# Kernel tuning notes

Hardware: AMD Instinct MI355X
Metric: run time of the kernel (lower is better)

Reference implementation:

```python
import jax, jax.numpy as jnp
import numpy as np

B, H, S, D = 4, 16, 2048, 128


def setup_inputs() -> dict:
    key = jax.random.key(0)
    kq, kk, kv = jax.random.split(key, 3)
    query = jax.random.normal(kq, (B, H, S, D), dtype=jnp.float32)
    key_t = jax.random.normal(kk, (B, H, S, D), dtype=jnp.float32)
    value = jax.random.normal(kv, (B, H, S, D), dtype=jnp.float32)
    # causal mask, broadcast over batch and heads: True = keep
    mask = jnp.tril(jnp.ones((S, S), dtype=bool))[None, None].repeat(B, 0).repeat(H, 1)
    return {"query": query, "key": key_t, "value": value, "mask": mask}


def reference(query, key, value, mask):
    scale = 1.0 / np.sqrt(D).astype(np.float32)
    # [b,h,sq,sk] scores
    scores = jnp.einsum("bhqd,bhkd->bhqk", query, key) * scale
    scores = jnp.where(mask, scores, -jnp.inf)
    probs = jax.nn.softmax(scores, axis=-1)
    return jnp.einsum("bhqk,bhkd->bhqd", probs, value)
```

## Files before the change

kernel.cpp:

```cpp
#include <hip/hip_runtime.h>


#define SLEN 2048
#define DDIM 128
#define NBH  64
#define QB   256
#define KB   64
#define NITEMS 512

typedef __bf16 bf16x8 __attribute__((ext_vector_type(8)));
typedef float  f32x16 __attribute__((ext_vector_type(16)));
typedef float  f32x4  __attribute__((ext_vector_type(4)));
typedef unsigned uint32x4 __attribute__((ext_vector_type(4)));
typedef unsigned short ushort_t;
typedef ushort_t ushort8 __attribute__((ext_vector_type(8)));

__device__ inline ushort_t f2bf(float f) {
  union { float f; unsigned u; } v; v.f = f;
  unsigned u = v.u;
  u += 0x7FFFu + ((u >> 16) & 1u);
  return (ushort_t)(u >> 16);
}

__device__ inline unsigned cvtpk_bf16(float lo, float hi) {
  unsigned r;
  asm("v_cvt_pk_bf16_f32 %0, %1, %2" : "=v"(r) : "v"(lo), "v"(hi));
  return r;
}

__device__ inline float exp2_fast(float x) {
  float r;
  asm("v_exp_f32 %0, %1" : "=v"(r) : "v"(x));
  return r;
}

__global__ __launch_bounds__(256) void prepass_kernel(
    const float* __restrict__ K, const float* __restrict__ V,
    ushort_t* __restrict__ Kb, ushort_t* __restrict__ Vt,
    int* __restrict__ cnt) {
  __shared__ float t[64][33];
  if (blockIdx.x == 0 && threadIdx.x == 0) *cnt = 0;
  if (blockIdx.x < 2048) {
    const int n4 = (int)((size_t)NBH * SLEN * DDIM / 4);
    const int stride = 2048 * 256;
    for (int i = blockIdx.x * 256 + threadIdx.x; i < n4; i += stride) {
      float4 x = reinterpret_cast<const float4*>(K)[i];
      unsigned lo = (unsigned)f2bf(x.x) | ((unsigned)f2bf(x.y) << 16);
      unsigned hi = (unsigned)f2bf(x.z) | ((unsigned)f2bf(x.w) << 16);
      reinterpret_cast<uint2*>(Kb)[i] = make_uint2(lo, hi);
    }
  } else {
    const int vb = (int)blockIdx.x - 2048;
    const int bh = vb >> 7;
    const int d0 = ((vb >> 5) & 3) * 32;
    const int s0 = (vb & 31) * 64;
    const int tx = threadIdx.x & 31;
    const int ty = threadIdx.x >> 5;
    const float* src = V + ((size_t)bh * SLEN + s0) * DDIM + d0;
#pragma unroll
    for (int j = 0; j < 8; ++j) {
      int sl = ty + j * 8;
      t[sl][tx] = src[(size_t)sl * DDIM + tx];
    }
    __syncthreads();
    ushort_t* dst = Vt + ((size_t)bh * DDIM + d0) * SLEN + s0;
#pragma unroll
    for (int j = 0; j < 4; ++j) {
      int dl = ty + j * 8;
      unsigned lo = f2bf(t[tx * 2][dl]);
      unsigned hi = f2bf(t[tx * 2 + 1][dl]);
      *reinterpret_cast<unsigned*>(&dst[(size_t)dl * SLEN + tx * 2]) =
          lo | (hi << 16);
    }
  }
}

__global__ __launch_bounds__(512, 1) void fattn11_kernel(
    const float* __restrict__ Q, const ushort_t* __restrict__ Kb,
    const ushort_t* __restrict__ Vt, float* __restrict__ Out,
    int* __restrict__ cnt) {
  __shared__ ushort_t K_sh[3][KB * DDIM];
  __shared__ ushort_t V_sh[3][DDIM * KB];
  __shared__ int item_sh;

  const int tid  = threadIdx.x;
  const int lane = tid & 63;
  const int wv   = tid >> 6;
  const int l31  = lane & 31;
  const int hi   = lane >> 5;

  const float qscale = 0.12751744f;
  const float THR = 11.0f;

  while (true) {
    if (tid == 0) item_sh = atomicAdd(cnt, 1);
    __syncthreads();
    const int item = item_sh;
    if (item >= NITEMS) break;

    const int qblk = 7 - (item >> 6);
    const int bh   = item & 63;

    const float*    Qp = Q  + (size_t)bh * SLEN * DDIM;
    const ushort_t* Kp = Kb + (size_t)bh * SLEN * DDIM;
    const ushort_t* Vp = Vt + (size_t)bh * DDIM * SLEN;
    float*          Op = Out + (size_t)bh * SLEN * DDIM;

    const int q0w = qblk * QB + wv * 32;
    const int qg  = q0w + l31;

    bf16x8 qf[8];
    {
      const float* qr = Qp + (size_t)qg * DDIM;
#pragma unroll
      for (int ds = 0; ds < 8; ++ds) {
        int d0 = ds * 16 + hi * 8;
        float4 x = *reinterpret_cast<const float4*>(qr + d0);
        float4 y = *reinterpret_cast<const float4*>(qr + d0 + 4);
        ushort8 uu;
        uu[0] = f2bf(x.x * qscale); uu[1] = f2bf(x.y * qscale);
        uu[2] = f2bf(x.z * qscale); uu[3] = f2bf(x.w * qscale);
        uu[4] = f2bf(y.x * qscale); uu[5] = f2bf(y.y * qscale);
        uu[6] = f2bf(y.z * qscale); uu[7] = f2bf(y.w * qscale);
        qf[ds] = __builtin_bit_cast(bf16x8, uu);
      }
    }

    f32x16 Oacc[4];
#pragma unroll
    for (int dt = 0; dt < 4; ++dt)
#pragma unroll
      for (int r = 0; r < 16; ++r) Oacc[dt][r] = 0.f;
    float m_run = -3.0e38f, l_run = 0.f;

    const int last_kb      = qblk * 4 + 3;
    const int last_kb_wave = (q0w + 31) >> 6;

    auto stage = [&](int buf, int kb) {
      const ushort_t* ksrc = Kp + (size_t)kb * KB * DDIM;
#pragma unroll
      for (int j = 0; j < 2; ++j) {
        int chunk = wv * 128 + j * 64 + lane;
        int row = chunk >> 4, c = chunk & 15;
        const ushort_t* g = ksrc + row * DDIM + ((c ^ (row & 7)) << 3);
        ushort_t* l = &K_sh[buf][(wv * 128 + j * 64) * 8];
        __builtin_amdgcn_global_load_lds(
            (const __attribute__((address_space(1))) unsigned*)g,
            (__attribute__((address_space(3))) unsigned*)l, 16, 0, 0);
      }
      const ushort_t* vsrc = Vp + (size_t)kb * KB;
#pragma unroll
      for (int j = 0; j < 2; ++j) {
        int chunk = wv * 128 + j * 64 + lane;
        int row = chunk >> 3, c = chunk & 7;
        const ushort_t* g = vsrc + (size_t)row * SLEN + ((c ^ (row & 7)) << 3);
        ushort_t* l = &V_sh[buf][(wv * 128 + j * 64) * 8];
        __builtin_amdgcn_global_load_lds(
            (const __attribute__((address_space(1))) unsigned*)g,
            (__attribute__((address_space(3))) unsigned*)l, 16, 0, 0);
      }
    };

    stage(0, 0);
    stage(1, 1);
    asm volatile("s_waitcnt vmcnt(4)" ::: "memory");
    __builtin_amdgcn_s_barrier();
    __builtin_amdgcn_sched_barrier(0);

    for (int kb = 0; kb <= last_kb; ++kb) {
      const int buf = kb % 3;
      const bool pf = (kb + 2 <= last_kb);
      if (pf) stage((kb + 2) % 3, kb + 2);

      if (kb <= last_kb_wave) {
        f32x16 sac[2];
#pragma unroll
        for (int mt = 0; mt < 2; ++mt) {
          f32x16 a;
#pragma unroll
          for (int r = 0; r < 16; ++r) a[r] = 0.f;
          int row = mt * 32 + l31;
          int sw = row & 7;
          __builtin_amdgcn_s_setprio(1);
#pragma unroll
          for (int ds = 0; ds < 8; ++ds) {
            int c = ds * 2 + hi;
            bf16x8 kf = *reinterpret_cast<const bf16x8*>(
                &K_sh[buf][row * DDIM + ((c ^ sw) << 3)]);
            a = __builtin_amdgcn_mfma_f32_32x32x16_bf16(kf, qf[ds], a, 0, 0, 0);
          }
          __builtin_amdgcn_s_setprio(0);
          sac[mt] = a;
        }

        if (kb * 64 + 63 > q0w) {
#pragma unroll
          for (int mt = 0; mt < 2; ++mt) {
            int kbase = kb * 64 + mt * 32 + 4 * hi;
#pragma unroll
            for (int r = 0; r < 16; ++r) {
              int krow = (r & 3) + 8 * (r >> 2);
              if (kbase + krow > qg) sac[mt][r] = -3.0e38f;
            }
          }
        }

        float p0 = sac[0][0], p1 = sac[0][1], p2 = sac[0][2], p3 = sac[0][3];
#pragma unroll
        for (int r = 4; r < 16; r += 4) {
          p0 = fmaxf(p0, sac[0][r + 0]); p1 = fmaxf(p1, sac[0][r + 1]);
          p2 = fmaxf(p2, sac[0][r + 2]); p3 = fmaxf(p3, sac[0][r + 3]);
        }
#pragma unroll
        for (int r = 0; r < 16; r += 4) {
          p0 = fmaxf(p0, sac[1][r + 0]); p1 = fmaxf(p1, sac[1][r + 1]);
          p2 = fmaxf(p2, sac[1][r + 2]); p3 = fmaxf(p3, sac[1][r + 3]);
        }
        float tm = fmaxf(fmaxf(p0, p1), fmaxf(p2, p3));
        tm = fmaxf(tm, __shfl_xor(tm, 32));

        if (!__all(tm - m_run <= THR)) {
          float mnew  = fmaxf(m_run, tm);
          float alpha = exp2_fast(m_run - mnew);
          m_run = mnew;
          l_run *= alpha;
#pragma unroll
          for (int dt = 0; dt < 4; ++dt)
#pragma unroll
            for (int r = 0; r < 16; ++r) Oacc[dt][r] *= alpha;
        }

        float s0 = 0.f, s1 = 0.f, s2 = 0.f, s3 = 0.f;
#pragma unroll
        for (int mt = 0; mt < 2; ++mt)
#pragma unroll
          for (int r = 0; r < 16; r += 4) {
            float e0 = exp2_fast(sac[mt][r + 0] - m_run);
            float e1 = exp2_fast(sac[mt][r + 1] - m_run);
            float e2 = exp2_fast(sac[mt][r + 2] - m_run);
            float e3 = exp2_fast(sac[mt][r + 3] - m_run);
            sac[mt][r + 0] = e0; sac[mt][r + 1] = e1;
            sac[mt][r + 2] = e2; sac[mt][r + 3] = e3;
            s0 += e0; s1 += e1; s2 += e2; s3 += e3;
          }
        float rs = (s0 + s1) + (s2 + s3);
        rs += __shfl_xor(rs, 32);
        l_run += rs;

        uint32x4 pw[4];
#pragma unroll
        for (int ks = 0; ks < 4; ++ks) {
          const int mt = ks >> 1;
          const int hb = 8 * (ks & 1);
          unsigned X  = cvtpk_bf16(sac[mt][hb + 0], sac[mt][hb + 1]);
          unsigned X2 = cvtpk_bf16(sac[mt][hb + 2], sac[mt][hb + 3]);
          unsigned Y  = cvtpk_bf16(sac[mt][hb + 4], sac[mt][hb + 5]);
          unsigned Y2 = cvtpk_bf16(sac[mt][hb + 6], sac[mt][hb + 7]);
          asm("v_permlane32_swap_b32 %0, %1" : "+v"(X),  "+v"(Y));
          asm("v_permlane32_swap_b32 %0, %1" : "+v"(X2), "+v"(Y2));
          uint32x4 f; f.x = X; f.y = X2; f.z = Y; f.w = Y2;
          pw[ks] = f;
        }

#pragma unroll
        for (int dt = 0; dt < 4; ++dt) {
          int row = dt * 32 + l31;
          int sw = row & 7;
          __builtin_amdgcn_s_setprio(1);
#pragma unroll
          for (int ks = 0; ks < 4; ++ks) {
            int c = ks * 2 + hi;
            bf16x8 vf = *reinterpret_cast<const bf16x8*>(
                &V_sh[buf][row * 64 + ((c ^ sw) << 3)]);
            Oacc[dt] = __builtin_amdgcn_mfma_f32_32x32x16_bf16(
                vf, __builtin_bit_cast(bf16x8, pw[ks]), Oacc[dt], 0, 0, 0);
          }
          __builtin_amdgcn_s_setprio(0);
        }
      }

      if (kb < last_kb) {
        if (pf) { asm volatile("s_waitcnt vmcnt(4)" ::: "memory"); }
        else    { asm volatile("s_waitcnt vmcnt(0)" ::: "memory"); }
        __builtin_amdgcn_s_barrier();
        __builtin_amdgcn_sched_barrier(0);
      }
    }

    {
      float invl = 1.0f / l_run;
      float* orow = Op + (size_t)qg * DDIM;
#pragma unroll
      for (int dt = 0; dt < 4; ++dt)
#pragma unroll
        for (int rq = 0; rq < 4; ++rq) {
          float4 o;
          o.x = Oacc[dt][rq * 4 + 0] * invl;
          o.y = Oacc[dt][rq * 4 + 1] * invl;
          o.z = Oacc[dt][rq * 4 + 2] * invl;
          o.w = Oacc[dt][rq * 4 + 3] * invl;
          int d = dt * 32 + 8 * rq + 4 * hi;
          *reinterpret_cast<float4*>(orow + d) = o;
        }
    }
    __syncthreads();
  }
}

__global__ __launch_bounds__(256) void fattn_kernel(
    const float* __restrict__ Q, const float* __restrict__ K,
    const float* __restrict__ V, float* __restrict__ Out) {
  __shared__ ushort_t Kf_sh[64 * 128];
  __shared__ ushort_t Vf_sh[128 * 64];
  __shared__ ushort_t P_sh[4][16 * 64];

  const int tid  = threadIdx.x;
  const int lane = tid & 63;
  const int wv   = tid >> 6;
  const int l16  = lane & 15;
  const int lhi  = lane >> 4;
  const int qblk = blockIdx.x;
  const int bh   = blockIdx.y;
  const float scale = 0.08838834764831845f;

  const size_t base = (size_t)bh * SLEN * DDIM;
  const float* Qp = Q + base;
  const float* Kp = K + base;
  const float* Vp = V + base;
  float*       Op = Out + base;

  bf16x8 qf[4];
  {
    const int qrow = qblk * 64 + wv * 16 + l16;
    const float* qr = Qp + (size_t)qrow * DDIM;
#pragma unroll
    for (int dc = 0; dc < 4; ++dc) {
      int d0 = dc * 32 + lhi * 8;
      float4 x = *reinterpret_cast<const float4*>(qr + d0);
      float4 y = *reinterpret_cast<const float4*>(qr + d0 + 4);
      ushort8 uu;
      uu[0] = f2bf(x.x * scale); uu[1] = f2bf(x.y * scale);
      uu[2] = f2bf(x.z * scale); uu[3] = f2bf(x.w * scale);
      uu[4] = f2bf(y.x * scale); uu[5] = f2bf(y.y * scale);
      uu[6] = f2bf(y.z * scale); uu[7] = f2bf(y.w * scale);
      qf[dc] = __builtin_bit_cast(bf16x8, uu);
    }
  }

  f32x4 Oacc[8];
#pragma unroll
  for (int i = 0; i < 8; ++i) Oacc[i] = (f32x4){0.f, 0.f, 0.f, 0.f};
  float m_run[4], l_run[4];
#pragma unroll
  for (int r = 0; r < 4; ++r) { m_run[r] = -3.0e38f; l_run[r] = 0.f; }

  for (int kb = 0; kb <= qblk; ++kb) {
    __syncthreads();
    {
      const float* src = Kp + (size_t)kb * 64 * DDIM;
#pragma unroll
      for (int it = 0; it < 8; ++it) {
        int idx4 = it * 256 + tid;
        int r  = idx4 >> 5;
        int c4 = idx4 & 31;
        float4 x = *reinterpret_cast<const float4*>(src + r * DDIM + c4 * 4);
        unsigned lo = ((unsigned)f2bf(x.y) << 16) | f2bf(x.x);
        unsigned hh = ((unsigned)f2bf(x.w) << 16) | f2bf(x.z);
        int e = (r * 128 + c4 * 4) ^ ((r & 7) << 3);
        *reinterpret_cast<uint2*>(&Kf_sh[e]) = make_uint2(lo, hh);
      }
      const float* vs = Vp + (size_t)kb * 64 * DDIM;
#pragma unroll
      for (int it = 0; it < 8; ++it) {
        int idx4 = it * 256 + tid;
        int r  = idx4 >> 5;
        int c4 = idx4 & 31;
        float4 x = *reinterpret_cast<const float4*>(vs + r * DDIM + c4 * 4);
        int c0 = c4 * 4;
        float vals[4] = {x.x, x.y, x.z, x.w};
#pragma unroll
        for (int j = 0; j < 4; ++j) {
          int d = c0 + j;
          Vf_sh[(d * 64 + r) ^ ((d & 7) << 3)] = f2bf(vals[j]);
        }
      }
    }
    __syncthreads();

    f32x4 sacc[4];
#pragma unroll
    for (int g = 0; g < 4; ++g) {
      f32x4 acc = (f32x4){0.f, 0.f, 0.f, 0.f};
#pragma unroll
      for (int dc = 0; dc < 4; ++dc) {
        int row = g * 16 + l16;
        int e = (row * 128 + dc * 32 + lhi * 8) ^ ((row & 7) << 3);
        bf16x8 kf = *reinterpret_cast<const bf16x8*>(&Kf_sh[e]);
        acc = __builtin_amdgcn_mfma_f32_16x16x32_bf16(qf[dc], kf, acc, 0, 0, 0);
      }
      sacc[g] = acc;
    }

    if (kb == qblk) {
      int q0 = lhi * 4;
#pragma unroll
      for (int g = 0; g < 4; ++g) {
        int kcol = g * 16 + l16;
#pragma unroll
        for (int r = 0; r < 4; ++r) {
          if (kcol > wv * 16 + q0 + r) sacc[g][r] = -3.0e38f;
        }
      }
    }

    float tmax[4];
#pragma unroll
    for (int r = 0; r < 4; ++r)
      tmax[r] = fmaxf(fmaxf(sacc[0][r], sacc[1][r]),
                      fmaxf(sacc[2][r], sacc[3][r]));
#pragma unroll
    for (int x = 1; x < 16; x <<= 1) {
#pragma unroll
      for (int r = 0; r < 4; ++r)
        tmax[r] = fmaxf(tmax[r], __shfl_xor(tmax[r], x));
    }

    float alpha[4], mnew[4];
#pragma unroll
    for (int r = 0; r < 4; ++r) {
      mnew[r]  = fmaxf(m_run[r], tmax[r]);
      alpha[r] = __expf(m_run[r] - mnew[r]);
      m_run[r] = mnew[r];
    }

    float rsum[4] = {0.f, 0.f, 0.f, 0.f};
#pragma unroll
    for (int g = 0; g < 4; ++g) {
#pragma unroll
      for (int r = 0; r < 4; ++r) {
        float p = __expf(sacc[g][r] - mnew[r]);
        rsum[r] += p;
        int prow = lhi * 4 + r;
        P_sh[wv][(prow * 64 + g * 16 + l16) ^ ((prow & 7) << 3)] = f2bf(p);
      }
    }
#pragma unroll
    for (int x = 1; x < 16; x <<= 1) {
#pragma unroll
      for (int r = 0; r < 4; ++r) rsum[r] += __shfl_xor(rsum[r], x);
    }
#pragma unroll
    for (int r = 0; r < 4; ++r) l_run[r] = l_run[r] * alpha[r] + rsum[r];

#pragma unroll
    for (int dg = 0; dg < 8; ++dg)
#pragma unroll
      for (int r = 0; r < 4; ++r) Oacc[dg][r] *= alpha[r];

    bf16x8 pf[2];
#pragma unroll
    for (int kc = 0; kc < 2; ++kc) {
      int e = (l16 * 64 + kc * 32 + lhi * 8) ^ ((l16 & 7) << 3);
      pf[kc] = *reinterpret_cast<const bf16x8*>(&P_sh[wv][e]);
    }
#pragma unroll
    for (int dg = 0; dg < 8; ++dg) {
#pragma unroll
      for (int kc = 0; kc < 2; ++kc) {
        int row = dg * 16 + l16;
        int e = (row * 64 + kc * 32 + lhi * 8) ^ ((row & 7) << 3);
        bf16x8 vf = *reinterpret_cast<const bf16x8*>(&Vf_sh[e]);
        Oacc[dg] = __builtin_amdgcn_mfma_f32_16x16x32_bf16(pf[kc], vf, Oacc[dg], 0, 0, 0);
      }
    }
  }

#pragma unroll
  for (int r = 0; r < 4; ++r) {
    float inv = 1.0f / l_run[r];
    int q = qblk * 64 + wv * 16 + lhi * 4 + r;
    float* orow = Op + (size_t)q * DDIM;
#pragma unroll
    for (int dg = 0; dg < 8; ++dg)
      orow[dg * 16 + l16] = Oacc[dg][r] * inv;
  }
}

extern "C" void kernel_launch(void* const* d_in, const int* in_sizes, int n_in,
                              void* d_out, int out_size, void* d_ws, size_t ws_size,
                              hipStream_t stream) {
  const float* Q = (const float*)d_in[0];
  const float* K = (const float*)d_in[1];
  const float* V = (const float*)d_in[2];
  float* O = (float*)d_out;

  const size_t n_elem = (size_t)NBH * SLEN * DDIM;
  const size_t need   = n_elem * 2 * 2 + 64;

  if (ws_size >= need) {
    ushort_t* Kbf = (ushort_t*)d_ws;
    ushort_t* Vt  = Kbf + n_elem;
    int* cnt      = (int*)(Vt + n_elem);
    prepass_kernel<<<2048 + 8192, 256, 0, stream>>>(K, V, Kbf, Vt, cnt);
    fattn11_kernel<<<dim3(NITEMS), dim3(512), 0, stream>>>(Q, Kbf, Vt, O, cnt);
  } else {
    fattn_kernel<<<dim3(SLEN / 64, NBH), dim3(256), 0, stream>>>(Q, K, V, O);
  }
}
```

Baseline: 141.0 us.

## Load K fragments directly into registers instead of staging through LDS

K tiles are no longer copied into shared memory. Each wave loads its own MFMA operand fragments for K from global memory straight into 16 vector registers, prefetching the next block right after the QK MFMAs. V keeps LDS staging, but with a double buffer instead of a triple buffer, and the vmcnt waits are retuned to match. This removes the LDS traffic and space used for K. In exchange, all 8 waves each re-read the same K block from global memory or cache, and the prefetch distance for V shrinks to one block, which risks higher register pressure and more exposed latency.

Result: slower. 208.8 us (+48.1%).

```diff
diff --git a/kernel.cpp b/kernel.cpp
--- a/kernel.cpp
+++ b/kernel.cpp
@@ -75,12 +75,11 @@
   }
 }
 
-__global__ __launch_bounds__(512, 1) void fattn11_kernel(
+__global__ __launch_bounds__(512, 1) void fattn12_kernel(
     const float* __restrict__ Q, const ushort_t* __restrict__ Kb,
     const ushort_t* __restrict__ Vt, float* __restrict__ Out,
     int* __restrict__ cnt) {
-  __shared__ ushort_t K_sh[3][KB * DDIM];
-  __shared__ ushort_t V_sh[3][DDIM * KB];
+  __shared__ ushort_t V_sh[2][DDIM * KB];
   __shared__ int item_sh;
 
   const int tid  = threadIdx.x;
@@ -136,18 +135,18 @@
     const int last_kb      = qblk * 4 + 3;
     const int last_kb_wave = (q0w + 31) >> 6;
 
-    auto stage = [&](int buf, int kb) {
+    bf16x8 kf[16];
+    auto kfetch = [&](int kb) {
       const ushort_t* ksrc = Kp + (size_t)kb * KB * DDIM;
 #pragma unroll
-      for (int j = 0; j < 2; ++j) {
-        int chunk = wv * 128 + j * 64 + lane;
-        int row = chunk >> 4, c = chunk & 15;
-        const ushort_t* g = ksrc + row * DDIM + ((c ^ (row & 7)) << 3);
-        ushort_t* l = &K_sh[buf][(wv * 128 + j * 64) * 8];
-        __builtin_amdgcn_global_load_lds(
-            (const __attribute__((address_space(1))) unsigned*)g,
-            (__attribute__((address_space(3))) unsigned*)l, 16, 0, 0);
-      }
+      for (int mt = 0; mt < 2; ++mt)
+#pragma unroll
+        for (int ds = 0; ds < 8; ++ds) {
+          const ushort_t* g = ksrc + (mt * 32 + l31) * DDIM + ds * 16 + hi * 8;
+          kf[mt * 8 + ds] = *reinterpret_cast<const bf16x8*>(g);
+        }
+    };
+    auto vstage = [&](int buf, int kb) {
       const ushort_t* vsrc = Vp + (size_t)kb * KB;
 #pragma unroll
       for (int j = 0; j < 2; ++j) {
@@ -161,16 +160,16 @@
       }
     };
 
-    stage(0, 0);
-    stage(1, 1);
-    asm volatile("s_waitcnt vmcnt(4)" ::: "memory");
+    vstage(0, 0);
+    kfetch(0);
+    asm volatile("s_waitcnt vmcnt(16)" ::: "memory");
     __builtin_amdgcn_s_barrier();
     __builtin_amdgcn_sched_barrier(0);
 
     for (int kb = 0; kb <= last_kb; ++kb) {
-      const int buf = kb % 3;
-      const bool pf = (kb + 2 <= last_kb);
-      if (pf) stage((kb + 2) % 3, kb + 2);
+      const int buf  = kb & 1;
+      const bool more = kb < last_kb;
+      if (more) vstage(buf ^ 1, kb + 1);
 
       if (kb <= last_kb_wave) {
         f32x16 sac[2];
@@ -179,19 +178,16 @@
           f32x16 a;
 #pragma unroll
           for (int r = 0; r < 16; ++r) a[r] = 0.f;
-          int row = mt * 32 + l31;
-          int sw = row & 7;
           __builtin_amdgcn_s_setprio(1);
 #pragma unroll
-          for (int ds = 0; ds < 8; ++ds) {
-            int c = ds * 2 + hi;
-            bf16x8 kf = *reinterpret_cast<const bf16x8*>(
-                &K_sh[buf][row * DDIM + ((c ^ sw) << 3)]);
-            a = __builtin_amdgcn_mfma_f32_32x32x16_bf16(kf, qf[ds], a, 0, 0, 0);
-          }
+          for (int ds = 0; ds < 8; ++ds)
+            a = __builtin_amdgcn_mfma_f32_32x32x16_bf16(
+                kf[mt * 8 + ds], qf[ds], a, 0, 0, 0);
           __builtin_amdgcn_s_setprio(0);
           sac[mt] = a;
         }
+
+        if (more) kfetch(kb + 1);
 
         if (kb * 64 + 63 > q0w) {
 #pragma unroll
@@ -277,11 +273,12 @@
           }
           __builtin_amdgcn_s_setprio(0);
         }
-      }
-
-      if (kb < last_kb) {
-        if (pf) { asm volatile("s_waitcnt vmcnt(4)" ::: "memory"); }
-        else    { asm volatile("s_waitcnt vmcnt(0)" ::: "memory"); }
+      } else {
+        if (more) kfetch(kb + 1);
+      }
+
+      if (more) {
+        asm volatile("s_waitcnt vmcnt(16)" ::: "memory");
         __builtin_amdgcn_s_barrier();
         __builtin_amdgcn_sched_barrier(0);
       }
@@ -502,7 +499,7 @@
     ushort_t* Vt  = Kbf + n_elem;
     int* cnt      = (int*)(Vt + n_elem);
     prepass_kernel<<<2048 + 8192, 256, 0, stream>>>(K, V, Kbf, Vt, cnt);
-    fattn11_kernel<<<dim3(NITEMS), dim3(512), 0, stream>>>(Q, Kbf, Vt, O, cnt);
+    fattn12_kernel<<<dim3(NITEMS), dim3(512), 0, stream>>>(Q, Kbf, Vt, O, cnt);
   } else {
     fattn_kernel<<<dim3(SLEN / 64, NBH), dim3(256), 0, stream>>>(Q, K, V, O);
   }
```
